# Optimization experiments

Measured on AMD Instinct MI355X. Metric: run time of the kernel, lower is better.

Reference implementation:

```python
import jax, jax.numpy as jnp
import numpy as np


def _ln(x, w, b, eps=1e-5):
    m = jnp.mean(x, -1, keepdims=True)
    v = jnp.mean((x - m) ** 2, -1, keepdims=True)
    return (x - m) / jnp.sqrt(v + eps) * w + b


def _l2norm(x, axis):
    n = jnp.sqrt(jnp.sum(x * x, axis=axis, keepdims=True))
    return x / jnp.maximum(n, 1e-12)


def _bilinear(img, gx, gy):
    # torch F.grid_sample, bilinear, align_corners=False, padding_mode='zeros'
    # img (B,C,H,W); gx, gy (B,N) in normalized [-1,1] coords -> out (B,C,N)
    B, C, H, W = img.shape
    x = ((gx + 1.0) * W - 1.0) * 0.5
    y = ((gy + 1.0) * H - 1.0) * 0.5
    x0f = jnp.floor(x)
    y0f = jnp.floor(y)
    wx1 = x - x0f
    wy1 = y - y0f
    x0 = x0f.astype(jnp.int32)
    y0 = y0f.astype(jnp.int32)
    imgf = img.reshape(B, C, H * W)

    def gat(xi, yi, wv):
        valid = (xi >= 0) & (xi < W) & (yi >= 0) & (yi < H)
        idx = jnp.clip(yi, 0, H - 1) * W + jnp.clip(xi, 0, W - 1)
        vals = jnp.take_along_axis(imgf, idx[:, None, :], axis=2)  # (B,C,N)
        return vals * (wv * valid)[:, None, :]

    return (gat(x0, y0, (1 - wx1) * (1 - wy1)) + gat(x0 + 1, y0, wx1 * (1 - wy1))
            + gat(x0, y0 + 1, (1 - wx1) * wy1) + gat(x0 + 1, y0 + 1, wx1 * wy1))


def _forward(xyz, g14d, v_feats, ext, intr, offsets,
             gate_w1, gate_b1, gate_w2, gate_b2,
             bn_w1, bn_b1, bn_w2, bn_b2, bn_ln_w, bn_ln_b,
             cw, cw2, hw, ln1_w, ln1_b, gw, gln_w, gln_b, mask):
    B, N, _ = xyz.shape
    BV, C, H, W = v_feats.shape
    V = BV // B
    vf = v_feats.reshape(B, V, C, H, W)
    gelu = lambda t: jax.nn.gelu(t, approximate=False)  # torch nn.GELU default

    # ---- PhysicsGatedProjection ----
    scale = jnp.clip(g14d[:, :, 4:7], 0.01, 10.0)
    opacity = jnp.clip(g14d[:, :, 11:12], 0.0, 1.0)
    gate = jax.nn.sigmoid(gelu(jnp.concatenate([scale, opacity], -1) @ gate_w1 + gate_b1) @ gate_w2 + gate_b2)  # (B,N,1)

    pts_homo = jnp.concatenate([xyz, jnp.ones((B, N, 1), xyz.dtype)], -1)  # (B,N,4)
    sum_f = jnp.zeros((B, N, 32), xyz.dtype)
    sum_m = jnp.zeros((B, N, 1), xyz.dtype)
    for v in range(V):  # small fixed view count
        cam = jnp.einsum('bij,bnj->bni', ext[:, v], pts_homo)      # (B,N,3)
        uvh = jnp.einsum('bij,bnj->bni', intr[:, v], cam)          # (B,N,3)
        depth = jnp.clip(uvh[:, :, 2:3], 1e-6, None)
        uv = uvh[:, :, :2] / depth
        grid = jnp.stack([2.0 * uv[:, :, 0] / (W * 14.0) - 1.0,
                          2.0 * uv[:, :, 1] / (H * 14.0) - 1.0], -1) + offsets  # (B,N,2)
        sampled = _bilinear(vf[:, v], grid[:, :, 0], grid[:, :, 1]).transpose(0, 2, 1)  # (B,N,C)
        h = gelu(sampled @ bn_w1 + bn_b1)
        v32 = _ln(h @ bn_w2 + bn_b2, bn_ln_w, bn_ln_b)             # (B,N,32)
        valid = (depth[:, :, 0] > 0.1) & jnp.all(jnp.abs(grid) <= 1.0, -1) & mask
        vm = valid[:, :, None].astype(xyz.dtype)
        sum_f = sum_f + v32 * gate * vm
        sum_m = sum_m + vm
    fused = sum_f / (sum_m + 1e-6)                                 # (B,N,32)

    # ---- NetVLADLoupe ----
    act = jax.nn.softmax(_ln(fused @ cw, ln1_w, ln1_b), -1)        # (B,N,K)
    act = act * mask[:, :, None].astype(fused.dtype)
    a_sum = jnp.sum(act, 1, keepdims=True)                         # (B,1,K)
    a = a_sum * cw2                                                # (B,D,K)
    vlad = jnp.einsum('bnk,bnd->bdk', act, fused) - a              # (B,D,K)
    vlad = _l2norm(vlad, axis=1)
    vlad = vlad.reshape(B, -1)
    vlad = _l2norm(vlad, axis=1)
    out = vlad @ hw                                                # (B,256)
    gates = jax.nn.sigmoid(_ln(out @ gw, gln_w, gln_b))
    return out * gates


def setup_inputs() -> dict:
    key = jax.random.key(0)
    ks = jax.random.split(key, 16)
    B, N, V, C, H, W = 4, 16384, 6, 384, 32, 32
    d = {}
    d['xyz'] = jax.random.normal(ks[0], (B, N, 3)) * 10.0
    d['g14d'] = jax.random.uniform(ks[1], (B, N, 14))
    d['v_feats'] = jax.random.normal(ks[2], (B * V, C, H, W))
    R = jnp.eye(3)[None, None] + 0.05 * jax.random.normal(ks[3], (B, V, 3, 3))
    t = jnp.concatenate([2.0 * jax.random.normal(ks[4], (B, V, 2, 1)),
                         20.0 + 5.0 * jax.random.uniform(ks[5], (B, V, 1, 1))], axis=2)
    d['ext'] = jnp.concatenate([R, t], -1)                          # (B,V,3,4)
    base_K = jnp.array([[200.0, 0.0, 224.0], [0.0, 200.0, 224.0], [0.0, 0.0, 1.0]])
    d['intr'] = base_K[None, None] + 2.0 * jax.random.normal(ks[6], (B, V, 3, 3)) * jnp.array([[1., 0., 1.], [0., 1., 1.], [0., 0., 0.]])
    d['offsets'] = jnp.zeros((B, N, 2))
    d['mask'] = jnp.ones((B, N), dtype=bool)
    # params
    d['gate_w1'] = jax.random.normal(ks[7], (4, 16)) * 0.5
    d['gate_b1'] = jnp.zeros((16,))
    d['gate_w2'] = jax.random.normal(ks[8], (16, 1)) * 0.25
    d['gate_b2'] = jnp.zeros((1,))
    d['bn_w1'] = jax.random.normal(ks[9], (384, 64)) / np.sqrt(384.0)
    d['bn_b1'] = jnp.zeros((64,))
    d['bn_w2'] = jax.random.normal(ks[10], (64, 32)) / 8.0
    d['bn_b2'] = jnp.zeros((32,))
    d['bn_ln_w'] = jnp.ones((32,))
    d['bn_ln_b'] = jnp.zeros((32,))
    d['cw'] = jax.random.normal(ks[11], (32, 64)) / np.sqrt(32.0)
    d['cw2'] = jax.random.normal(ks[12], (1, 32, 64)) / np.sqrt(32.0)
    d['hw'] = jax.random.normal(ks[13], (32 * 64, 256)) / np.sqrt(32.0)
    d['ln1_w'] = jnp.ones((64,))
    d['ln1_b'] = jnp.zeros((64,))
    d['gw'] = jax.random.normal(ks[14], (256, 256)) / 16.0
    d['gln_w'] = jnp.ones((256,))
    d['gln_b'] = jnp.zeros((256,))
    return d


def reference(xyz, g14d, v_feats, ext, intr, offsets, mask,
              gate_w1, gate_b1, gate_w2, gate_b2,
              bn_w1, bn_b1, bn_w2, bn_b2, bn_ln_w, bn_ln_b,
              cw, cw2, hw, ln1_w, ln1_b, gw, gln_w, gln_b):
    return _forward(xyz, g14d, v_feats, ext, intr, offsets,
                    gate_w1, gate_b1, gate_w2, gate_b2,
                    bn_w1, bn_b1, bn_w2, bn_b2, bn_ln_w, bn_ln_b,
                    cw, cw2, hw, ln1_w, ln1_b, gw, gln_w, gln_b, mask)
```

## Files before the change

### kernel.cpp

```cpp
#include <hip/hip_runtime.h>
#include <hip/hip_bf16.h>
#include <math.h>

#define B_ 4
#define N_ 16384
#define V_ 6
#define C_ 384
#define H_ 32
#define W_ 32
#define HW_ 1024
#define BN_ (B_ * N_)

__device__ __forceinline__ float gelu_f(float x){
  return 0.5f * x * (1.0f + erff(x * 0.70710678118654752440f));
}
__device__ __forceinline__ float sigmoid_f(float x){
  return 1.0f / (1.0f + expf(-x));
}
__device__ __forceinline__ float wsum64(float v){
  #pragma unroll
  for (int m = 1; m < 64; m <<= 1) v += __shfl_xor(v, m);
  return v;
}
__device__ __forceinline__ float wmax64(float v){
  #pragma unroll
  for (int m = 1; m < 64; m <<= 1) v = fmaxf(v, __shfl_xor(v, m));
  return v;
}
__device__ __forceinline__ float wsum32(float v){
  #pragma unroll
  for (int m = 1; m < 32; m <<= 1) v += __shfl_xor(v, m);
  return v;
}

__global__ __launch_bounds__(512) void k0_proj(
    const float* __restrict__ vf, const float* __restrict__ w1,
    float* __restrict__ proj)
{
  const int bv  = blockIdx.x >> 5;
  const int px0 = (blockIdx.x & 31) << 5;
  __shared__ float fs[64][32];
  const int t = threadIdx.x;
  const int j = t & 63;
  const int pg = t >> 6;
  const int sc = t >> 3, sq = t & 7;
  float acc0 = 0.f, acc1 = 0.f, acc2 = 0.f, acc3 = 0.f;

  for (int c0 = 0; c0 < C_; c0 += 64){
    const float4 sv = *(const float4*)&vf[((size_t)bv * C_ + c0 + sc) * HW_
                                          + px0 + sq * 4];
    __syncthreads();
    *(float4*)&fs[sc][sq * 4] = sv;
    __syncthreads();
    for (int c = 0; c < 64; ++c){
      const float w = w1[(c0 + c) * 64 + j];
      const float4 hv = *(const float4*)&fs[c][pg * 4];
      acc0 += hv.x * w;
      acc1 += hv.y * w;
      acc2 += hv.z * w;
      acc3 += hv.w * w;
    }
  }
  const size_t ob = ((size_t)bv * HW_ + px0 + pg * 4) * 64 + j;
  proj[ob]           = acc0;
  proj[ob + 64]      = acc1;
  proj[ob + 128]     = acc2;
  proj[ob + 192]     = acc3;
}

__global__ __launch_bounds__(256) void k1a_records(
    const float* __restrict__ xyz, const float* __restrict__ g14d,
    const float* __restrict__ ext, const float* __restrict__ intr,
    const float* __restrict__ offs, const unsigned char* __restrict__ mask,
    const float* __restrict__ gw1, const float* __restrict__ gb1,
    const float* __restrict__ gw2, const float* __restrict__ gb2,
    float4* __restrict__ rec2, float* __restrict__ gate_g,
    float* __restrict__ summ_g)
{
  const int p = blockIdx.x * 256 + threadIdx.x;
  const int b = p >> 14;

  const float* g = g14d + (size_t)p * 14;
  float in0 = fminf(fmaxf(g[4],  0.01f), 10.f);
  float in1 = fminf(fmaxf(g[5],  0.01f), 10.f);
  float in2 = fminf(fmaxf(g[6],  0.01f), 10.f);
  float in3 = fminf(fmaxf(g[11], 0.0f),  1.f);
  float gacc = gb2[0];
  #pragma unroll
  for (int hh = 0; hh < 16; ++hh){
    float tv = gb1[hh] + in0 * gw1[hh] + in1 * gw1[16 + hh]
             + in2 * gw1[32 + hh] + in3 * gw1[48 + hh];
    gacc += gelu_f(tv) * gw2[hh];
  }
  gate_g[p] = sigmoid_f(gacc);

  const float px = xyz[p * 3], py = xyz[p * 3 + 1], pz = xyz[p * 3 + 2];
  const float offx = offs[p * 2], offy = offs[p * 2 + 1];
  const float mval = mask[p] ? 1.f : 0.f;

  float summ = 0.f;
  #pragma unroll
  for (int v = 0; v < V_; ++v){
    const float* E = ext  + (size_t)(b * V_ + v) * 12;
    const float* I = intr + (size_t)(b * V_ + v) * 9;
    float c0 = E[0]*px + E[1]*py + E[2]*pz + E[3];
    float c1 = E[4]*px + E[5]*py + E[6]*pz + E[7];
    float c2 = E[8]*px + E[9]*py + E[10]*pz + E[11];
    float u0 = I[0]*c0 + I[1]*c1 + I[2]*c2;
    float u1 = I[3]*c0 + I[4]*c1 + I[5]*c2;
    float u2 = I[6]*c0 + I[7]*c1 + I[8]*c2;
    float depth = fmaxf(u2, 1e-6f);
    float gx = 2.0f * (u0 / depth) / (W_ * 14.0f) - 1.0f + offx;
    float gy = 2.0f * (u1 / depth) / (H_ * 14.0f) - 1.0f + offy;
    float fx = ((gx + 1.0f) * W_ - 1.0f) * 0.5f;
    float fy = ((gy + 1.0f) * H_ - 1.0f) * 0.5f;
    fx = fminf(fmaxf(fx, -4.0f), 36.0f);
    fy = fminf(fmaxf(fy, -4.0f), 36.0f);
    float fx0 = floorf(fx), fy0 = floorf(fy);
    float wx = fx - fx0, wy = fy - fy0;
    int x0 = (int)fx0, y0 = (int)fy0;
    float v00 = (float)((x0 >= 0 && x0 < W_) && (y0 >= 0 && y0 < H_));
    float v10 = (float)((x0 + 1 >= 0 && x0 + 1 < W_) && (y0 >= 0 && y0 < H_));
    float v01 = (float)((x0 >= 0 && x0 < W_) && (y0 + 1 >= 0 && y0 + 1 < H_));
    float v11 = (float)((x0 + 1 >= 0 && x0 + 1 < W_) && (y0 + 1 >= 0 && y0 + 1 < H_));
    float vm = (depth > 0.1f && fabsf(gx) <= 1.0f && fabsf(gy) <= 1.0f) ? mval : 0.f;
    summ += vm;
    const int x0c = min(max(x0, 0), W_ - 1), x1c = min(max(x0 + 1, 0), W_ - 1);
    const int y0c = min(max(y0, 0), H_ - 1), y1c = min(max(y0 + 1, 0), H_ - 1);
    float4 wv;
    wv.x = (1.f - wx) * (1.f - wy) * v00;
    wv.y = wx * (1.f - wy) * v10;
    wv.z = (1.f - wx) * wy * v01;
    wv.w = wx * wy * v11;
    int4 iv;
    iv.x = (y0c * W_ + x0c) | ((vm > 0.f ? 1 : 0) << 16);
    iv.y = y0c * W_ + x1c;
    iv.z = y1c * W_ + x0c;
    iv.w = y1c * W_ + x1c;
    const size_t ri = 2 * ((size_t)v * BN_ + p);
    rec2[ri] = wv;
    rec2[ri + 1] = *(const float4*)&iv;
  }
  summ_g[p] = summ;
}

__global__ __launch_bounds__(256) void k1b_points(
    const float4* __restrict__ rec2, const float* __restrict__ gate_g,
    const float* __restrict__ summ_g, const unsigned char* __restrict__ mask,
    const float* __restrict__ proj,
    const float* __restrict__ b1, const float* __restrict__ w2,
    const float* __restrict__ b2, const float* __restrict__ lnw,
    const float* __restrict__ lnb, const float* __restrict__ cw,
    const float* __restrict__ ln1w, const float* __restrict__ ln1b,
    float* __restrict__ fused_out, float* __restrict__ act_out)
{
  __shared__ float h_s[4][V_][64];
  __shared__ float fu_s[4][32];
  const int wave = threadIdx.x >> 6, lane = threadIdx.x & 63;
  const int p = (blockIdx.x << 2) + wave;
  const int b = p >> 14;
  const int d = lane & 31, half = lane >> 5;

  float w2c[32];
  #pragma unroll
  for (int j = 0; j < 32; ++j) w2c[j] = w2[(half * 32 + j) * 32 + d];
  const float b1v = b1[lane], b2v = b2[d], lnwv = lnw[d], lnbv = lnb[d];
  const float gate = gate_g[p];
  const float summ = summ_g[p];
  const float mval = mask[p] ? 1.f : 0.f;
  const unsigned vbase = (unsigned)(b * V_) * (HW_ * 64) + (unsigned)lane;

  float hv[V_], vmf[V_];
  #pragma unroll
  for (int v = 0; v < V_; ++v){
    const size_t ri = 2 * ((size_t)v * BN_ + p);
    const float4 wv = rec2[ri];
    const float4 ivf = rec2[ri + 1];
    const int4 iv = *(const int4*)&ivf;
    vmf[v] = (float)(iv.x >> 16);
    const unsigned vb = vbase + (unsigned)(v * HW_ * 64);
    float s = wv.x * proj[vb + ((unsigned)(iv.x & 0xFFFF) << 6)];
    s      += wv.y * proj[vb + ((unsigned)iv.y << 6)];
    s      += wv.z * proj[vb + ((unsigned)iv.z << 6)];
    s      += wv.w * proj[vb + ((unsigned)iv.w << 6)];
    hv[v] = gelu_f(s + b1v);
  }
  #pragma unroll
  for (int v = 0; v < V_; ++v) h_s[wave][v][lane] = hv[v];
  asm volatile("" ::: "memory");
  float yp[V_];
  #pragma unroll
  for (int v = 0; v < V_; ++v){
    const float4* hp = reinterpret_cast<const float4*>(&h_s[wave][v][half * 32]);
    float y = 0.f;
    #pragma unroll
    for (int q = 0; q < 8; ++q){
      const float4 hq = hp[q];
      y += hq.x * w2c[4 * q + 0];
      y += hq.y * w2c[4 * q + 1];
      y += hq.z * w2c[4 * q + 2];
      y += hq.w * w2c[4 * q + 3];
    }
    yp[v] = y;
  }
  float sum_f = 0.f;
  #pragma unroll
  for (int v = 0; v < V_; ++v){
    float yv = yp[v] + __shfl_xor(yp[v], 32) + b2v;
    float mean = wsum32(yv) * (1.f / 32.f);
    float dv = yv - mean;
    float var = wsum32(dv * dv) * (1.f / 32.f);
    float v32 = dv * rsqrtf(var + 1e-5f) * lnwv + lnbv;
    sum_f += v32 * gate * vmf[v];
  }
  const float fu = sum_f / (summ + 1e-6f);
  if (lane < 32){
    fu_s[wave][lane] = fu;
    fused_out[(size_t)p * 32 + lane] = fu;
  }
  asm volatile("" ::: "memory");

  const float4* fp = reinterpret_cast<const float4*>(&fu_s[wave][0]);
  float z = 0.f;
  #pragma unroll
  for (int q = 0; q < 8; ++q){
    const float4 fv = fp[q];
    z += fv.x * cw[(4 * q + 0) * 64 + lane];
    z += fv.y * cw[(4 * q + 1) * 64 + lane];
    z += fv.z * cw[(4 * q + 2) * 64 + lane];
    z += fv.w * cw[(4 * q + 3) * 64 + lane];
  }
  float mean = wsum64(z) * (1.f / 64.f);
  float dz = z - mean;
  float var = wsum64(dz * dz) * (1.f / 64.f);
  float zl = dz * rsqrtf(var + 1e-5f) * ln1w[lane] + ln1b[lane];
  float mx = wmax64(zl);
  float e = expf(zl - mx);
  float ssum = wsum64(e);
  act_out[(size_t)p * 64 + lane] = (e / ssum) * mval;
}

__global__ __launch_bounds__(256) void k2_vlad(
    const float* __restrict__ fused, const float* __restrict__ act,
    float* __restrict__ vlad_acc, float* __restrict__ asum_acc)
{
  __shared__ float act_s[64][64];
  __shared__ float fu_s[64][32];
  const int b = blockIdx.x >> 6, seg = blockIdx.x & 63;
  const int n0 = seg * 256;
  const int t = threadIdx.x, k = t & 63, dg = t >> 6;
  float vacc[8];
  #pragma unroll
  for (int r = 0; r < 8; ++r) vacc[r] = 0.f;
  float asum = 0.f;

  for (int sc = 0; sc < 4; ++sc){
    int nb = n0 + sc * 64;
    #pragma unroll
    for (int i = 0; i < 16; ++i){
      int idx = t + i * 256;
      act_s[idx >> 6][idx & 63] =
        act[((size_t)((b << 14) + nb + (idx >> 6))) * 64 + (idx & 63)];
    }
    #pragma unroll
    for (int i = 0; i < 8; ++i){
      int idx = t + i * 256;
      fu_s[idx >> 5][idx & 31] =
        fused[((size_t)((b << 14) + nb + (idx >> 5))) * 32 + (idx & 31)];
    }
    __syncthreads();
    for (int i = 0; i < 64; ++i){
      float a = act_s[i][k];
      const float* fr = &fu_s[i][dg * 8];
      #pragma unroll
      for (int r = 0; r < 8; ++r) vacc[r] += a * fr[r];
      if (dg == 0) asum += a;
    }
    __syncthreads();
  }
  #pragma unroll
  for (int r = 0; r < 8; ++r)
    atomicAdd(&vlad_acc[b * 2048 + (dg * 8 + r) * 64 + k], vacc[r]);
  if (dg == 0) atomicAdd(&asum_acc[b * 64 + k], asum);
}

__global__ __launch_bounds__(256) void k3a_norm(
    const float* __restrict__ vlad_acc, const float* __restrict__ asum_acc,
    const float* __restrict__ cw2, float* __restrict__ vs1_g,
    float* __restrict__ ginv_g)
{
  const int b = blockIdx.x, t = threadIdx.x;
  __shared__ float vs[2048];
  __shared__ float denom[64];
  __shared__ float redA[4];
  #pragma unroll
  for (int i = 0; i < 8; ++i){
    int idx = t + i * 256;
    vs[idx] = vlad_acc[b * 2048 + idx]
            - asum_acc[b * 64 + (idx & 63)] * cw2[idx];
  }
  __syncthreads();
  if (t < 64){
    float ss = 0.f;
    #pragma unroll
    for (int dd = 0; dd < 32; ++dd){ float x = vs[dd * 64 + t]; ss += x * x; }
    denom[t] = fmaxf(sqrtf(ss), 1e-12f);
  }
  __syncthreads();
  float ls = 0.f;
  #pragma unroll
  for (int i = 0; i < 8; ++i){
    int idx = t + i * 256;
    float x = vs[idx] / denom[idx & 63];
    vs1_g[b * 2048 + idx] = x;
    ls += x * x;
  }
  ls = wsum64(ls);
  if ((t & 63) == 0) redA[t >> 6] = ls;
  __syncthreads();
  if (t == 0){
    float tot = redA[0] + redA[1] + redA[2] + redA[3];
    ginv_g[b] = 1.0f / fmaxf(sqrtf(tot), 1e-12f);
  }
}

__global__ __launch_bounds__(256) void k3b_hw(
    const float* __restrict__ vs1_g, const float* __restrict__ hw,
    float* __restrict__ out_acc)
{
  const int b = blockIdx.x >> 3, ks = blockIdx.x & 7;
  const int t = threadIdx.x;
  __shared__ float xs[256];
  xs[t] = vs1_g[b * 2048 + ks * 256 + t];
  __syncthreads();
  float acc = 0.f;
  #pragma unroll 4
  for (int i = 0; i < 256; ++i)
    acc += xs[i] * hw[(size_t)(ks * 256 + i) * 256 + t];
  atomicAdd(&out_acc[b * 256 + t], acc);
}

__global__ __launch_bounds__(256) void k3c_gate(
    const float* __restrict__ out_acc, const float* __restrict__ ginv_g,
    const float* __restrict__ gww, const float* __restrict__ glnw,
    const float* __restrict__ glnb, float* __restrict__ outp)
{
  const int b = blockIdx.x, t = threadIdx.x;
  __shared__ float out_s[256];
  __shared__ float redB[4], redC[4];
  const float ginv = ginv_g[b];
  const float o = out_acc[b * 256 + t] * ginv;
  out_s[t] = o;
  __syncthreads();
  float gp = 0.f;
  #pragma unroll 4
  for (int i = 0; i < 256; ++i) gp += out_s[i] * gww[i * 256 + t];
  float s1 = wsum64(gp);
  if ((t & 63) == 0) redB[t >> 6] = s1;
  __syncthreads();
  float mean = (redB[0] + redB[1] + redB[2] + redB[3]) * (1.f / 256.f);
  float dv = gp - mean;
  float s2 = wsum64(dv * dv);
  if ((t & 63) == 0) redC[t >> 6] = s2;
  __syncthreads();
  float var = (redC[0] + redC[1] + redC[2] + redC[3]) * (1.f / 256.f);
  float gt = sigmoid_f(dv * rsqrtf(var + 1e-5f) * glnw[t] + glnb[t]);
  outp[b * 256 + t] = o * gt;
}

extern "C" void kernel_launch(void* const* d_in, const int* in_sizes, int n_in,
                              void* d_out, int out_size, void* d_ws, size_t ws_size,
                              hipStream_t stream)
{
  (void)in_sizes; (void)n_in; (void)out_size; (void)ws_size;
  const float* xyz   = (const float*)d_in[0];
  const float* g14d  = (const float*)d_in[1];
  const float* vf    = (const float*)d_in[2];
  const float* ext   = (const float*)d_in[3];
  const float* intr  = (const float*)d_in[4];
  const float* offs  = (const float*)d_in[5];
  const unsigned char* mask = (const unsigned char*)d_in[6];
  const float* gw1   = (const float*)d_in[7];
  const float* gb1   = (const float*)d_in[8];
  const float* gw2   = (const float*)d_in[9];
  const float* gb2   = (const float*)d_in[10];
  const float* bnw1  = (const float*)d_in[11];
  const float* bnb1  = (const float*)d_in[12];
  const float* bnw2  = (const float*)d_in[13];
  const float* bnb2  = (const float*)d_in[14];
  const float* bnlnw = (const float*)d_in[15];
  const float* bnlnb = (const float*)d_in[16];
  const float* cw    = (const float*)d_in[17];
  const float* cw2   = (const float*)d_in[18];
  const float* hw    = (const float*)d_in[19];
  const float* ln1w  = (const float*)d_in[20];
  const float* ln1b  = (const float*)d_in[21];
  const float* gww   = (const float*)d_in[22];
  const float* glnw  = (const float*)d_in[23];
  const float* glnb  = (const float*)d_in[24];

  char* ws = (char*)d_ws;
  float* vlad_acc = (float*)(ws);
  float* asum_acc = (float*)(ws + 32768);
  float* proj     = (float*)(ws + 33792);
  float* fusedb   = (float*)(ws + 6325248);
  float* actb     = (float*)(ws + 14713856);
  float4* rec2    = (float4*)(ws + 31491072);
  float* gate_g   = (float*)(ws + 44073472);
  float* summ_g   = (float*)(ws + 44335616);
  float* ginv_g   = (float*)(ws + 31491072);
  float* vs1_g    = (float*)(ws + 31491328);
  float* out_acc  = (float*)(ws + 31524096);

  hipMemsetAsync(d_ws, 0, 33792, stream);
  k0_proj    <<<dim3(768),   dim3(512), 0, stream>>>(vf, bnw1, proj);
  k1a_records<<<dim3(256),   dim3(256), 0, stream>>>(
      xyz, g14d, ext, intr, offs, mask, gw1, gb1, gw2, gb2,
      rec2, gate_g, summ_g);
  k1b_points <<<dim3(16384), dim3(256), 0, stream>>>(
      rec2, gate_g, summ_g, mask, proj,
      bnb1, bnw2, bnb2, bnlnw, bnlnb, cw, ln1w, ln1b, fusedb, actb);
  k2_vlad    <<<dim3(B_ * 64), dim3(256), 0, stream>>>(fusedb, actb, vlad_acc, asum_acc);
  hipMemsetAsync(ws + 31524096, 0, 4096, stream);
  k3a_norm   <<<dim3(B_),    dim3(256), 0, stream>>>(vlad_acc, asum_acc, cw2,
                                                     vs1_g, ginv_g);
  k3b_hw     <<<dim3(32),    dim3(256), 0, stream>>>(vs1_g, hw, out_acc);
  k3c_gate   <<<dim3(B_),    dim3(256), 0, stream>>>(out_acc, ginv_g, gww,
                                                     glnw, glnb, (float*)d_out);
}
```

Baseline: 375.0 us.

## Fuse projection-record and per-point kernels into one thread-per-point kernel

Merges the record-building kernel and the per-point MLP/LayerNorm/softmax kernel into a single kernel where each thread handles one point end to end. The per-view bilinear gather, 64->32 MLP, LayerNorm, cluster projection and softmax now run in registers, with weights read as uniform loads. This removes the intermediate record, gate and mask-count buffers along with their global traffic and one launch. In exchange it drops from wave-per-point to thread-per-point, which means heavy register use, only 1024 single-wave blocks, and uncoalesced row gathers from proj.

```diff
diff --git a/kernel.cpp b/kernel.cpp
--- a/kernel.cpp
+++ b/kernel.cpp
@@ -20,16 +20,6 @@
 __device__ __forceinline__ float wsum64(float v){
   #pragma unroll
   for (int m = 1; m < 64; m <<= 1) v += __shfl_xor(v, m);
-  return v;
-}
-__device__ __forceinline__ float wmax64(float v){
-  #pragma unroll
-  for (int m = 1; m < 64; m <<= 1) v = fmaxf(v, __shfl_xor(v, m));
-  return v;
-}
-__device__ __forceinline__ float wsum32(float v){
-  #pragma unroll
-  for (int m = 1; m < 32; m <<= 1) v += __shfl_xor(v, m);
   return v;
 }
 
@@ -68,17 +58,22 @@
   proj[ob + 192]     = acc3;
 }
 
-__global__ __launch_bounds__(256) void k1a_records(
+__global__ __launch_bounds__(64) void k1_fused(
     const float* __restrict__ xyz, const float* __restrict__ g14d,
     const float* __restrict__ ext, const float* __restrict__ intr,
     const float* __restrict__ offs, const unsigned char* __restrict__ mask,
     const float* __restrict__ gw1, const float* __restrict__ gb1,
     const float* __restrict__ gw2, const float* __restrict__ gb2,
-    float4* __restrict__ rec2, float* __restrict__ gate_g,
-    float* __restrict__ summ_g)
-{
-  const int p = blockIdx.x * 256 + threadIdx.x;
+    const float* __restrict__ proj,
+    const float* __restrict__ b1, const float* __restrict__ w2,
+    const float* __restrict__ b2, const float* __restrict__ lnw,
+    const float* __restrict__ lnb, const float* __restrict__ cw,
+    const float* __restrict__ ln1w, const float* __restrict__ ln1b,
+    float* __restrict__ fused_out, float* __restrict__ act_out)
+{
+  const int p = blockIdx.x * 64 + threadIdx.x;
   const int b = p >> 14;
+  const int bu = __builtin_amdgcn_readfirstlane(b);
 
   const float* g = g14d + (size_t)p * 14;
   float in0 = fminf(fmaxf(g[4],  0.01f), 10.f);
@@ -92,17 +87,21 @@
              + in2 * gw1[32 + hh] + in3 * gw1[48 + hh];
     gacc += gelu_f(tv) * gw2[hh];
   }
-  gate_g[p] = sigmoid_f(gacc);
+  const float gate = sigmoid_f(gacc);
 
   const float px = xyz[p * 3], py = xyz[p * 3 + 1], pz = xyz[p * 3 + 2];
   const float offx = offs[p * 2], offy = offs[p * 2 + 1];
   const float mval = mask[p] ? 1.f : 0.f;
 
+  float sum_f[32];
+  #pragma unroll
+  for (int d = 0; d < 32; ++d) sum_f[d] = 0.f;
   float summ = 0.f;
-  #pragma unroll
+
+  #pragma unroll 1
   for (int v = 0; v < V_; ++v){
-    const float* E = ext  + (size_t)(b * V_ + v) * 12;
-    const float* I = intr + (size_t)(b * V_ + v) * 9;
+    const float* E = ext  + (size_t)(bu * V_ + v) * 12;
+    const float* I = intr + (size_t)(bu * V_ + v) * 9;
     float c0 = E[0]*px + E[1]*py + E[2]*pz + E[3];
     float c1 = E[4]*px + E[5]*py + E[6]*pz + E[7];
     float c2 = E[8]*px + E[9]*py + E[10]*pz + E[11];
@@ -127,117 +126,104 @@
     summ += vm;
     const int x0c = min(max(x0, 0), W_ - 1), x1c = min(max(x0 + 1, 0), W_ - 1);
     const int y0c = min(max(y0, 0), H_ - 1), y1c = min(max(y0 + 1, 0), H_ - 1);
-    float4 wv;
-    wv.x = (1.f - wx) * (1.f - wy) * v00;
-    wv.y = wx * (1.f - wy) * v10;
-    wv.z = (1.f - wx) * wy * v01;
-    wv.w = wx * wy * v11;
-    int4 iv;
-    iv.x = (y0c * W_ + x0c) | ((vm > 0.f ? 1 : 0) << 16);
-    iv.y = y0c * W_ + x1c;
-    iv.z = y1c * W_ + x0c;
-    iv.w = y1c * W_ + x1c;
-    const size_t ri = 2 * ((size_t)v * BN_ + p);
-    rec2[ri] = wv;
-    rec2[ri + 1] = *(const float4*)&iv;
-  }
-  summ_g[p] = summ;
-}
-
-__global__ __launch_bounds__(256) void k1b_points(
-    const float4* __restrict__ rec2, const float* __restrict__ gate_g,
-    const float* __restrict__ summ_g, const unsigned char* __restrict__ mask,
-    const float* __restrict__ proj,
-    const float* __restrict__ b1, const float* __restrict__ w2,
-    const float* __restrict__ b2, const float* __restrict__ lnw,
-    const float* __restrict__ lnb, const float* __restrict__ cw,
-    const float* __restrict__ ln1w, const float* __restrict__ ln1b,
-    float* __restrict__ fused_out, float* __restrict__ act_out)
-{
-  __shared__ float h_s[4][V_][64];
-  __shared__ float fu_s[4][32];
-  const int wave = threadIdx.x >> 6, lane = threadIdx.x & 63;
-  const int p = (blockIdx.x << 2) + wave;
-  const int b = p >> 14;
-  const int d = lane & 31, half = lane >> 5;
-
-  float w2c[32];
-  #pragma unroll
-  for (int j = 0; j < 32; ++j) w2c[j] = w2[(half * 32 + j) * 32 + d];
-  const float b1v = b1[lane], b2v = b2[d], lnwv = lnw[d], lnbv = lnb[d];
-  const float gate = gate_g[p];
-  const float summ = summ_g[p];
-  const float mval = mask[p] ? 1.f : 0.f;
-  const unsigned vbase = (unsigned)(b * V_) * (HW_ * 64) + (unsigned)lane;
-
-  float hv[V_], vmf[V_];
-  #pragma unroll
-  for (int v = 0; v < V_; ++v){
-    const size_t ri = 2 * ((size_t)v * BN_ + p);
-    const float4 wv = rec2[ri];
-    const float4 ivf = rec2[ri + 1];
-    const int4 iv = *(const int4*)&ivf;
-    vmf[v] = (float)(iv.x >> 16);
-    const unsigned vb = vbase + (unsigned)(v * HW_ * 64);
-    float s = wv.x * proj[vb + ((unsigned)(iv.x & 0xFFFF) << 6)];
-    s      += wv.y * proj[vb + ((unsigned)iv.y << 6)];
-    s      += wv.z * proj[vb + ((unsigned)iv.z << 6)];
-    s      += wv.w * proj[vb + ((unsigned)iv.w << 6)];
-    hv[v] = gelu_f(s + b1v);
-  }
-  #pragma unroll
-  for (int v = 0; v < V_; ++v) h_s[wave][v][lane] = hv[v];
-  asm volatile("" ::: "memory");
-  float yp[V_];
-  #pragma unroll
-  for (int v = 0; v < V_; ++v){
-    const float4* hp = reinterpret_cast<const float4*>(&h_s[wave][v][half * 32]);
-    float y = 0.f;
-    #pragma unroll
-    for (int q = 0; q < 8; ++q){
-      const float4 hq = hp[q];
-      y += hq.x * w2c[4 * q + 0];
-      y += hq.y * w2c[4 * q + 1];
-      y += hq.z * w2c[4 * q + 2];
-      y += hq.w * w2c[4 * q + 3];
-    }
-    yp[v] = y;
-  }
-  float sum_f = 0.f;
-  #pragma unroll
-  for (int v = 0; v < V_; ++v){
-    float yv = yp[v] + __shfl_xor(yp[v], 32) + b2v;
-    float mean = wsum32(yv) * (1.f / 32.f);
-    float dv = yv - mean;
-    float var = wsum32(dv * dv) * (1.f / 32.f);
-    float v32 = dv * rsqrtf(var + 1e-5f) * lnwv + lnbv;
-    sum_f += v32 * gate * vmf[v];
-  }
-  const float fu = sum_f / (summ + 1e-6f);
-  if (lane < 32){
-    fu_s[wave][lane] = fu;
-    fused_out[(size_t)p * 32 + lane] = fu;
-  }
-  asm volatile("" ::: "memory");
-
-  const float4* fp = reinterpret_cast<const float4*>(&fu_s[wave][0]);
-  float z = 0.f;
+    const float wv0 = (1.f - wx) * (1.f - wy) * v00;
+    const float wv1 = wx * (1.f - wy) * v10;
+    const float wv2 = (1.f - wx) * wy * v01;
+    const float wv3 = wx * wy * v11;
+    const float* pr = proj + (size_t)(bu * V_ + v) * (HW_ * 64);
+    const float* t00p = pr + (y0c * W_ + x0c) * 64;
+    const float* t10p = pr + (y0c * W_ + x1c) * 64;
+    const float* t01p = pr + (y1c * W_ + x0c) * 64;
+    const float* t11p = pr + (y1c * W_ + x1c) * 64;
+
+    float y[32];
+    #pragma unroll
+    for (int d = 0; d < 32; ++d) y[d] = 0.f;
+    #pragma unroll
+    for (int q = 0; q < 16; ++q){
+      const float4 a0 = *(const float4*)(t00p + q * 4);
+      const float4 a1 = *(const float4*)(t10p + q * 4);
+      const float4 a2 = *(const float4*)(t01p + q * 4);
+      const float4 a3 = *(const float4*)(t11p + q * 4);
+      float s0 = wv0 * a0.x; s0 += wv1 * a1.x; s0 += wv2 * a2.x; s0 += wv3 * a3.x;
+      float s1 = wv0 * a0.y; s1 += wv1 * a1.y; s1 += wv2 * a2.y; s1 += wv3 * a3.y;
+      float s2 = wv0 * a0.z; s2 += wv1 * a1.z; s2 += wv2 * a2.z; s2 += wv3 * a3.z;
+      float s3 = wv0 * a0.w; s3 += wv1 * a1.w; s3 += wv2 * a2.w; s3 += wv3 * a3.w;
+      const float h0 = gelu_f(s0 + b1[q * 4 + 0]);
+      const float h1 = gelu_f(s1 + b1[q * 4 + 1]);
+      const float h2 = gelu_f(s2 + b1[q * 4 + 2]);
+      const float h3 = gelu_f(s3 + b1[q * 4 + 3]);
+      #pragma unroll
+      for (int d = 0; d < 32; ++d) y[d] += h0 * w2[(q * 4 + 0) * 32 + d];
+      #pragma unroll
+      for (int d = 0; d < 32; ++d) y[d] += h1 * w2[(q * 4 + 1) * 32 + d];
+      #pragma unroll
+      for (int d = 0; d < 32; ++d) y[d] += h2 * w2[(q * 4 + 2) * 32 + d];
+      #pragma unroll
+      for (int d = 0; d < 32; ++d) y[d] += h3 * w2[(q * 4 + 3) * 32 + d];
+    }
+    float mean = 0.f;
+    #pragma unroll
+    for (int d = 0; d < 32; ++d){ y[d] += b2[d]; mean += y[d]; }
+    mean *= (1.f / 32.f);
+    float var = 0.f;
+    #pragma unroll
+    for (int d = 0; d < 32; ++d){ float dv = y[d] - mean; var += dv * dv; }
+    var *= (1.f / 32.f);
+    const float rinv = rsqrtf(var + 1e-5f);
+    #pragma unroll
+    for (int d = 0; d < 32; ++d){
+      float v32 = (y[d] - mean) * rinv * lnw[d] + lnb[d];
+      sum_f[d] += v32 * gate * vm;
+    }
+  }
+
+  const float rden = 1.f / (summ + 1e-6f);
+  float fu[32];
+  #pragma unroll
+  for (int d = 0; d < 32; ++d) fu[d] = sum_f[d] * rden;
   #pragma unroll
   for (int q = 0; q < 8; ++q){
-    const float4 fv = fp[q];
-    z += fv.x * cw[(4 * q + 0) * 64 + lane];
-    z += fv.y * cw[(4 * q + 1) * 64 + lane];
-    z += fv.z * cw[(4 * q + 2) * 64 + lane];
-    z += fv.w * cw[(4 * q + 3) * 64 + lane];
-  }
-  float mean = wsum64(z) * (1.f / 64.f);
-  float dz = z - mean;
-  float var = wsum64(dz * dz) * (1.f / 64.f);
-  float zl = dz * rsqrtf(var + 1e-5f) * ln1w[lane] + ln1b[lane];
-  float mx = wmax64(zl);
-  float e = expf(zl - mx);
-  float ssum = wsum64(e);
-  act_out[(size_t)p * 64 + lane] = (e / ssum) * mval;
+    float4 st;
+    st.x = fu[q * 4 + 0]; st.y = fu[q * 4 + 1];
+    st.z = fu[q * 4 + 2]; st.w = fu[q * 4 + 3];
+    *(float4*)&fused_out[(size_t)p * 32 + q * 4] = st;
+  }
+
+  float z[64];
+  #pragma unroll
+  for (int k = 0; k < 64; ++k) z[k] = 0.f;
+  #pragma unroll
+  for (int d = 0; d < 32; ++d){
+    const float fd = fu[d];
+    #pragma unroll
+    for (int k = 0; k < 64; ++k) z[k] += fd * cw[d * 64 + k];
+  }
+  float mean = 0.f;
+  #pragma unroll
+  for (int k = 0; k < 64; ++k) mean += z[k];
+  mean *= (1.f / 64.f);
+  float var = 0.f;
+  #pragma unroll
+  for (int k = 0; k < 64; ++k){ float dz = z[k] - mean; var += dz * dz; }
+  var *= (1.f / 64.f);
+  const float rinv = rsqrtf(var + 1e-5f);
+  #pragma unroll
+  for (int k = 0; k < 64; ++k) z[k] = (z[k] - mean) * rinv * ln1w[k] + ln1b[k];
+  float mx = z[0];
+  #pragma unroll
+  for (int k = 1; k < 64; ++k) mx = fmaxf(mx, z[k]);
+  float ssum = 0.f;
+  #pragma unroll
+  for (int k = 0; k < 64; ++k){ z[k] = expf(z[k] - mx); ssum += z[k]; }
+  const float rs = 1.f / ssum;
+  #pragma unroll
+  for (int q = 0; q < 16; ++q){
+    float4 st;
+    st.x = (z[q * 4 + 0] * rs) * mval; st.y = (z[q * 4 + 1] * rs) * mval;
+    st.z = (z[q * 4 + 2] * rs) * mval; st.w = (z[q * 4 + 3] * rs) * mval;
+    *(float4*)&act_out[(size_t)p * 64 + q * 4] = st;
+  }
 }
 
 __global__ __launch_bounds__(256) void k2_vlad(
@@ -402,29 +388,22 @@
   char* ws = (char*)d_ws;
   float* vlad_acc = (float*)(ws);
   float* asum_acc = (float*)(ws + 32768);
-  float* proj     = (float*)(ws + 33792);
-  float* fusedb   = (float*)(ws + 6325248);
-  float* actb     = (float*)(ws + 14713856);
-  float4* rec2    = (float4*)(ws + 31491072);
-  float* gate_g   = (float*)(ws + 44073472);
-  float* summ_g   = (float*)(ws + 44335616);
-  float* ginv_g   = (float*)(ws + 31491072);
-  float* vs1_g    = (float*)(ws + 31491328);
-  float* out_acc  = (float*)(ws + 31524096);
-
-  hipMemsetAsync(d_ws, 0, 33792, stream);
-  k0_proj    <<<dim3(768),   dim3(512), 0, stream>>>(vf, bnw1, proj);
-  k1a_records<<<dim3(256),   dim3(256), 0, stream>>>(
-      xyz, g14d, ext, intr, offs, mask, gw1, gb1, gw2, gb2,
-      rec2, gate_g, summ_g);
-  k1b_points <<<dim3(16384), dim3(256), 0, stream>>>(
-      rec2, gate_g, summ_g, mask, proj,
+  float* out_acc  = (float*)(ws + 33792);
+  float* ginv_g   = (float*)(ws + 37888);
+  float* proj     = (float*)(ws + 38912);
+  float* fusedb   = (float*)(ws + 6330368);
+  float* actb     = (float*)(ws + 14718976);
+  float* vs1_g    = (float*)(ws + 31496192);
+
+  hipMemsetAsync(d_ws, 0, 37888, stream);
+  k0_proj  <<<dim3(768),  dim3(512), 0, stream>>>(vf, bnw1, proj);
+  k1_fused <<<dim3(1024), dim3(64),  0, stream>>>(
+      xyz, g14d, ext, intr, offs, mask, gw1, gb1, gw2, gb2, proj,
       bnb1, bnw2, bnb2, bnlnw, bnlnb, cw, ln1w, ln1b, fusedb, actb);
-  k2_vlad    <<<dim3(B_ * 64), dim3(256), 0, stream>>>(fusedb, actb, vlad_acc, asum_acc);
-  hipMemsetAsync(ws + 31524096, 0, 4096, stream);
-  k3a_norm   <<<dim3(B_),    dim3(256), 0, stream>>>(vlad_acc, asum_acc, cw2,
-                                                     vs1_g, ginv_g);
-  k3b_hw     <<<dim3(32),    dim3(256), 0, stream>>>(vs1_g, hw, out_acc);
-  k3c_gate   <<<dim3(B_),    dim3(256), 0, stream>>>(out_acc, ginv_g, gww,
-                                                     glnw, glnb, (float*)d_out);
-}
+  k2_vlad  <<<dim3(B_ * 64), dim3(256), 0, stream>>>(fusedb, actb, vlad_acc, asum_acc);
+  k3a_norm <<<dim3(B_),   dim3(256), 0, stream>>>(vlad_acc, asum_acc, cw2,
+                                                  vs1_g, ginv_g);
+  k3b_hw   <<<dim3(32),   dim3(256), 0, stream>>>(vs1_g, hw, out_acc);
+  k3c_gate <<<dim3(B_),   dim3(256), 0, stream>>>(out_acc, ginv_g, gww,
+                                                  glnw, glnb, (float*)d_out);
+}
```

Measured after the change: 415.2 us. +10.7%, slower.
